# Performance work log

Measured on AMD Instinct MI355X. Metric: run time of the kernel, lower is better.

## Reference

```python
import jax, jax.numpy as jnp
import numpy as np

OUTPUT_SIZE = 256  # D: softmax / reduction dim (init arg output_size)


def setup_inputs() -> dict:
    key = jax.random.key(0)
    k1, k2 = jax.random.split(key)
    S = jax.random.normal(k1, (8192, OUTPUT_SIZE), dtype=jnp.float32)
    V = jax.random.normal(k2, (8192, OUTPUT_SIZE), dtype=jnp.float32)
    return {"S": S, "V": V}


def reference(S, V):
    # Original torch module: S, V viewed to (-1, D); for each pair (i, j)
    # it runs an online-softmax (flash-attention style) recurrence over D,
    # computing O[i, j] = sum_k softmax(S[i])_k * V[j, k].
    # Vectorized: O = softmax(S, -1) @ V.T  -> shape [N, M]
    D = S.shape[-1]
    S2 = S.reshape(-1, D)  # [N, D]
    V2 = V.reshape(-1, D)  # [M, D]
    P = jax.nn.softmax(S2, axis=-1)  # stable online-softmax equivalent
    return jnp.einsum('nd,md->nm', P, V2)
```

## Files before the change

kernel.cpp:

```cpp
#include <hip/hip_runtime.h>

typedef __attribute__((ext_vector_type(8))) short bf16x8;
typedef __attribute__((ext_vector_type(4))) float f32x4;

#define D_DIM 256
#define NROW  8192

__device__ __forceinline__ unsigned short f2bf(float x) {
  unsigned int u = __float_as_uint(x);
  u += 0x7fffu + ((u >> 16) & 1u);
  return (unsigned short)(u >> 16);
}

__device__ __forceinline__ void gload_lds16(const void* g, void* l) {
  __builtin_amdgcn_global_load_lds((__attribute__((address_space(1))) void*)g,
                                   (__attribute__((address_space(3))) void*)l,
                                   16, 0, 0);
}

__global__ __launch_bounds__(256) void softmax_rows(const float* __restrict__ S,
                                                    unsigned short* __restrict__ P) {
  const int row  = blockIdx.x * 4 + (threadIdx.x >> 6);
  const int lane = threadIdx.x & 63;
  float4 v = ((const float4*)(S + row * D_DIM))[lane];
  float m = fmaxf(fmaxf(v.x, v.y), fmaxf(v.z, v.w));
#pragma unroll
  for (int off = 32; off > 0; off >>= 1) m = fmaxf(m, __shfl_xor(m, off));
  float e0 = __expf(v.x - m), e1 = __expf(v.y - m);
  float e2 = __expf(v.z - m), e3 = __expf(v.w - m);
  float s = e0 + e1 + e2 + e3;
#pragma unroll
  for (int off = 32; off > 0; off >>= 1) s += __shfl_xor(s, off);
  const float inv = 1.0f / s;
  ushort4 o;
  o.x = f2bf(e0 * inv); o.y = f2bf(e1 * inv);
  o.z = f2bf(e2 * inv); o.w = f2bf(e3 * inv);
  ((ushort4*)(P + row * D_DIM))[lane] = o;
}

__global__ __launch_bounds__(256) void cast_v(const float* __restrict__ V,
                                              unsigned short* __restrict__ Vb) {
  const int i = blockIdx.x * 256 + threadIdx.x;
  float4 v = ((const float4*)V)[i];
  ushort4 o;
  o.x = f2bf(v.x); o.y = f2bf(v.y); o.z = f2bf(v.z); o.w = f2bf(v.w);
  ((ushort4*)Vb)[i] = o;
}

__global__ __launch_bounds__(256, 4) void gemm_bt(const unsigned short* __restrict__ P,
                                                  const unsigned short* __restrict__ Vb,
                                                  float* __restrict__ O) {
  __shared__ unsigned short smem[16384];

  const int t    = threadIdx.x;
  const int lane = t & 63;
  const int wave = t >> 6;
  const int wm   = (wave & 1) * 64;
  const int wn   = (wave >> 1) * 64;

  const int id  = blockIdx.x;
  const int xcd = id & 7;
  const int q   = id >> 3;
  const int bm  = xcd * 8 + (q & 7);
  const int bn  = q >> 3;

  f32x4 acc[4][4] = {};

  const int srow = t >> 2;
  const int xg   = (((t & 3) ^ ((srow >> 1) & 3)) * 8);
  const unsigned short* ga = P  + (size_t)(bm * 128 + srow) * D_DIM + xg;
  const unsigned short* gb = Vb + (size_t)(bn * 128 + srow) * D_DIM + xg;
  unsigned short* l0 = smem + t * 8;

  const int arow = wm + (lane & 15);
  const int brow = wn + (lane & 15);
  const int kch  = lane >> 4;

  {
    gload_lds16(ga, l0);
    gload_lds16(ga + 64 * D_DIM, l0 + 2048);
    gload_lds16(gb, l0 + 4096);
    gload_lds16(gb + 64 * D_DIM, l0 + 6144);
    asm volatile("s_waitcnt vmcnt(0)" ::: "memory");
    __builtin_amdgcn_s_barrier();
    __builtin_amdgcn_sched_barrier(0);
  }

#pragma unroll
  for (int tk = 0; tk < 8; ++tk) {
    const unsigned short* cur = smem + (tk & 1) * 8192;
    unsigned short*       nxt = l0 + ((tk & 1) ^ 1) * 8192;
    if (tk < 7) {
      const int ko = (tk + 1) * 32;
      gload_lds16(ga + ko,               nxt);
      gload_lds16(ga + 64 * D_DIM + ko,  nxt + 2048);
      gload_lds16(gb + ko,               nxt + 4096);
      gload_lds16(gb + 64 * D_DIM + ko,  nxt + 6144);
    }
    bf16x8 af[4], bfr[4];
#pragma unroll
    for (int mi = 0; mi < 4; ++mi) {
      const int r = arow + mi * 16;
      af[mi] = *(const bf16x8*)&cur[r * 32 + ((kch ^ ((r >> 1) & 3)) * 8)];
    }
#pragma unroll
    for (int ni = 0; ni < 4; ++ni) {
      const int r = brow + ni * 16;
      bfr[ni] = *(const bf16x8*)&cur[4096 + r * 32 + ((kch ^ ((r >> 1) & 3)) * 8)];
    }
#pragma unroll
    for (int mi = 0; mi < 4; ++mi)
#pragma unroll
      for (int ni = 0; ni < 4; ++ni)
        acc[mi][ni] = __builtin_amdgcn_mfma_f32_16x16x32_bf16(af[mi], bfr[ni],
                                                              acc[mi][ni], 0, 0, 0);
    if (tk < 7) {
      asm volatile("s_waitcnt vmcnt(0)" ::: "memory");
      __builtin_amdgcn_s_barrier();
      __builtin_amdgcn_sched_barrier(0);
    }
  }

  __syncthreads();

  float* smf = (float*)smem;
  float* ep  = smf + wave * 1088;
  const int qrow = (lane >> 4) * 4;
  const int qcol = lane & 15;
  const size_t orow0 = (size_t)(bm * 128 + wm);
  const int    ocol0 = bn * 128 + wn + (lane & 15) * 4;

#pragma unroll
  for (int mi = 0; mi < 4; ++mi) {
#pragma unroll
    for (int ni = 0; ni < 4; ++ni)
#pragma unroll
      for (int r = 0; r < 4; ++r)
        ep[(qrow + r) * 68 + ni * 16 + qcol] = acc[mi][ni][r];
#pragma unroll
    for (int qq = 0; qq < 4; ++qq) {
      const int rl = qq * 4 + (lane >> 4);
      f32x4 vv = *(const f32x4*)&ep[rl * 68 + (lane & 15) * 4];
      __builtin_nontemporal_store(vv,
          (f32x4*)&O[(orow0 + mi * 16 + rl) * NROW + ocol0]);
    }
  }
}

extern "C" void kernel_launch(void* const* d_in, const int* in_sizes, int n_in,
                              void* d_out, int out_size, void* d_ws, size_t ws_size,
                              hipStream_t stream) {
  const float* S = (const float*)d_in[0];
  const float* V = (const float*)d_in[1];
  float* O = (float*)d_out;

  unsigned short* P  = (unsigned short*)d_ws;
  unsigned short* Vb = P + (size_t)NROW * D_DIM;

  softmax_rows<<<NROW / 4, 256, 0, stream>>>(S, P);
  cast_v<<<(NROW * D_DIM / 4) / 256, 256, 0, stream>>>(V, Vb);
  gemm_bt<<<NROW / 128 * (NROW / 128), 256, 0, stream>>>(P, Vb, O);
}
```

Measured before the change: 289.4 us.

## Reshape GEMM block tile to 64x256 with 32x128 per-wave tiles

Changes the GEMM block tile from 128x128 to 64 rows by 256 columns. Each wave now computes 32x128 with a 2x8 MFMA accumulator grid, streaming B fragments one at a time. The epilogue writes 128-float-wide output rows, giving wider contiguous stores to the large fp32 output, and the XCD-aware block mapping is reworked to match. The cost is a less balanced wave tile: two A fragments against eight B fragments raises LDS reads per MFMA, and the LDS footprint grows.

```diff
diff --git a/kernel.cpp b/kernel.cpp
--- a/kernel.cpp
+++ b/kernel.cpp
@@ -50,37 +50,38 @@
 __global__ __launch_bounds__(256, 4) void gemm_bt(const unsigned short* __restrict__ P,
                                                   const unsigned short* __restrict__ Vb,
                                                   float* __restrict__ O) {
-  __shared__ unsigned short smem[16384];
+  __shared__ unsigned short smem[20480];
 
   const int t    = threadIdx.x;
   const int lane = t & 63;
   const int wave = t >> 6;
-  const int wm   = (wave & 1) * 64;
-  const int wn   = (wave >> 1) * 64;
+  const int wrow = (wave & 1) * 32;
+  const int wcol = (wave >> 1) * 128;
 
   const int id  = blockIdx.x;
   const int xcd = id & 7;
   const int q   = id >> 3;
-  const int bm  = xcd * 8 + (q & 7);
-  const int bn  = q >> 3;
+  const int bn  = xcd * 4 + (q & 3);
+  const int bm  = q >> 2;
 
-  f32x4 acc[4][4] = {};
+  f32x4 acc[2][8] = {};
 
   const int srow = t >> 2;
   const int xg   = (((t & 3) ^ ((srow >> 1) & 3)) * 8);
-  const unsigned short* ga = P  + (size_t)(bm * 128 + srow) * D_DIM + xg;
-  const unsigned short* gb = Vb + (size_t)(bn * 128 + srow) * D_DIM + xg;
-  unsigned short* l0 = smem + t * 8;
+  const unsigned short* ga = P  + (size_t)(bm * 64  + srow) * D_DIM + xg;
+  const unsigned short* gb = Vb + (size_t)(bn * 256 + srow) * D_DIM + xg;
 
-  const int arow = wm + (lane & 15);
-  const int brow = wn + (lane & 15);
+  const int arow = wrow + (lane & 15);
+  const int brow = wcol + (lane & 15);
   const int kch  = lane >> 4;
 
   {
-    gload_lds16(ga, l0);
-    gload_lds16(ga + 64 * D_DIM, l0 + 2048);
-    gload_lds16(gb, l0 + 4096);
-    gload_lds16(gb + 64 * D_DIM, l0 + 6144);
+    unsigned short* lA = smem + t * 8;
+    unsigned short* lB = smem + 2048 + t * 8;
+    gload_lds16(ga, lA);
+#pragma unroll
+    for (int s = 0; s < 4; ++s)
+      gload_lds16(gb + s * 64 * D_DIM, lB + s * 2048);
     asm volatile("s_waitcnt vmcnt(0)" ::: "memory");
     __builtin_amdgcn_s_barrier();
     __builtin_amdgcn_sched_barrier(0);
@@ -88,32 +89,30 @@
 
 #pragma unroll
   for (int tk = 0; tk < 8; ++tk) {
-    const unsigned short* cur = smem + (tk & 1) * 8192;
-    unsigned short*       nxt = l0 + ((tk & 1) ^ 1) * 8192;
+    const unsigned short* cur = smem + (tk & 1) * 10240;
+    unsigned short*       nb  = smem + ((tk & 1) ^ 1) * 10240;
     if (tk < 7) {
       const int ko = (tk + 1) * 32;
-      gload_lds16(ga + ko,               nxt);
-      gload_lds16(ga + 64 * D_DIM + ko,  nxt + 2048);
-      gload_lds16(gb + ko,               nxt + 4096);
-      gload_lds16(gb + 64 * D_DIM + ko,  nxt + 6144);
+      gload_lds16(ga + ko, nb + t * 8);
+#pragma unroll
+      for (int s = 0; s < 4; ++s)
+        gload_lds16(gb + s * 64 * D_DIM + ko, nb + 2048 + s * 2048 + t * 8);
     }
-    bf16x8 af[4], bfr[4];
+    bf16x8 af[2];
 #pragma unroll
-    for (int mi = 0; mi < 4; ++mi) {
+    for (int mi = 0; mi < 2; ++mi) {
       const int r = arow + mi * 16;
       af[mi] = *(const bf16x8*)&cur[r * 32 + ((kch ^ ((r >> 1) & 3)) * 8)];
     }
 #pragma unroll
-    for (int ni = 0; ni < 4; ++ni) {
+    for (int ni = 0; ni < 8; ++ni) {
       const int r = brow + ni * 16;
-      bfr[ni] = *(const bf16x8*)&cur[4096 + r * 32 + ((kch ^ ((r >> 1) & 3)) * 8)];
+      bf16x8 bfr = *(const bf16x8*)&cur[2048 + r * 32 + ((kch ^ ((r >> 1) & 3)) * 8)];
+      acc[0][ni] = __builtin_amdgcn_mfma_f32_16x16x32_bf16(af[0], bfr,
+                                                           acc[0][ni], 0, 0, 0);
+      acc[1][ni] = __builtin_amdgcn_mfma_f32_16x16x32_bf16(af[1], bfr,
+                                                           acc[1][ni], 0, 0, 0);
     }
-#pragma unroll
-    for (int mi = 0; mi < 4; ++mi)
-#pragma unroll
-      for (int ni = 0; ni < 4; ++ni)
-        acc[mi][ni] = __builtin_amdgcn_mfma_f32_16x16x32_bf16(af[mi], bfr[ni],
-                                                              acc[mi][ni], 0, 0, 0);
     if (tk < 7) {
       asm volatile("s_waitcnt vmcnt(0)" ::: "memory");
       __builtin_amdgcn_s_barrier();
@@ -124,23 +123,23 @@
   __syncthreads();
 
   float* smf = (float*)smem;
-  float* ep  = smf + wave * 1088;
+  float* ep  = smf + wave * 2112;
   const int qrow = (lane >> 4) * 4;
   const int qcol = lane & 15;
-  const size_t orow0 = (size_t)(bm * 128 + wm);
-  const int    ocol0 = bn * 128 + wn + (lane & 15) * 4;
+  const size_t orow0 = (size_t)(bm * 64 + wrow);
+  const int    ocol0 = bn * 256 + wcol + (lane & 31) * 4;
 
 #pragma unroll
-  for (int mi = 0; mi < 4; ++mi) {
+  for (int mi = 0; mi < 2; ++mi) {
 #pragma unroll
-    for (int ni = 0; ni < 4; ++ni)
+    for (int ni = 0; ni < 8; ++ni)
 #pragma unroll
       for (int r = 0; r < 4; ++r)
-        ep[(qrow + r) * 68 + ni * 16 + qcol] = acc[mi][ni][r];
+        ep[(qrow + r) * 132 + ni * 16 + qcol] = acc[mi][ni][r];
 #pragma unroll
-    for (int qq = 0; qq < 4; ++qq) {
-      const int rl = qq * 4 + (lane >> 4);
-      f32x4 vv = *(const f32x4*)&ep[rl * 68 + (lane & 15) * 4];
+    for (int it = 0; it < 8; ++it) {
+      const int rl = it * 2 + (lane >> 5);
+      f32x4 vv = *(const f32x4*)&ep[rl * 132 + (lane & 31) * 4];
       __builtin_nontemporal_store(vv,
           (f32x4*)&O[(orow0 + mi * 16 + rl) * NROW + ocol0]);
     }
@@ -159,5 +158,5 @@
 
   softmax_rows<<<NROW / 4, 256, 0, stream>>>(S, P);
   cast_v<<<(NROW * D_DIM / 4) / 256, 256, 0, stream>>>(V, Vb);
-  gemm_bt<<<NROW / 128 * (NROW / 128), 256, 0, stream>>>(P, Vb, O);
+  gemm_bt<<<(NROW / 64) * (NROW / 256), 256, 0, stream>>>(P, Vb, O);
 }
```

New measurement: 292.4 us. Within noise of the previous version (+1.0%).
